# Kernel tuning notes

Hardware: AMD Instinct MI355X
Metric: run time of the kernel (lower is better)

## Reference

```python
import jax, jax.numpy as jnp
import numpy as np

B = 262144          # batch of sample points
L = 16              # hash levels
T = 1 << 19         # hash table size per level
F = 2               # features per level
BASE_RES = 16
FINEST_RES = 512
DH = 64             # density MLP hidden
DOUT = 16           # density MLP out (density_out dim)
CH = 64             # color MLP hidden
PRIMES = np.array([1, 2654435761, 805459861], dtype=np.uint32)
_b = np.exp((np.log(FINEST_RES) - np.log(BASE_RES)) / (L - 1))
RES = jnp.asarray(np.floor(BASE_RES * _b ** np.arange(L)).astype(np.float32))  # (L,)


def _linear_init(key, fan_in, fan_out):
    kw, kb = jax.random.split(key)
    bound = 1.0 / np.sqrt(fan_in)
    w = jax.random.uniform(kw, (fan_in, fan_out), minval=-bound, maxval=bound)
    b = jax.random.uniform(kb, (fan_out,), minval=-bound, maxval=bound)
    return w, b


def setup_inputs() -> dict:
    key = jax.random.key(0)
    ks = jax.random.split(key, 10)
    coords = jax.random.uniform(ks[0], (B, 3), dtype=jnp.float32)          # in [0,1]
    directions = jax.random.normal(ks[1], (B, 3), dtype=jnp.float32)
    embeddings = jax.random.uniform(ks[2], (L, T, F), minval=-1e-4, maxval=1e-4, dtype=jnp.float32)
    dw1, db1 = _linear_init(ks[3], L * F, DH)
    dw2, db2 = _linear_init(ks[4], DH, DOUT)
    cw1, cb1 = _linear_init(ks[5], 16 + DOUT, CH)
    cw2, cb2 = _linear_init(ks[6], CH, CH)
    cw3, cb3 = _linear_init(ks[7], CH, CH)
    cw4, cb4 = _linear_init(ks[8], CH, 3)
    return dict(coords=coords, directions=directions, embeddings=embeddings,
                dw1=dw1, db1=db1, dw2=dw2, db2=db2,
                cw1=cw1, cb1=cb1, cw2=cw2, cb2=cb2,
                cw3=cw3, cb3=cb3, cw4=cw4, cb4=cb4)


def hash_encode(coords, embeddings):
    # coords: (B,3) in [0,1]; embeddings: (L,T,F)
    pos = coords[:, None, :] * RES[None, :, None]            # (B,L,3)
    p0 = jnp.floor(pos)
    frac = pos - p0                                           # (B,L,3)
    p0 = p0.astype(jnp.uint32)
    corners = jnp.stack([p0, p0 + jnp.uint32(1)], axis=-1)    # (B,L,3,2)
    h_ax = corners * jnp.asarray(PRIMES)[None, None, :, None]  # uint32 wraparound
    hidx = (h_ax[:, :, 0, :, None, None]
            ^ h_ax[:, :, 1, None, :, None]
            ^ h_ax[:, :, 2, None, None, :])                   # (B,L,2,2,2)
    hidx = (hidx & jnp.uint32(T - 1)).reshape(coords.shape[0], L, 8).astype(jnp.int32)
    feats = embeddings[jnp.arange(L)[None, :, None], hidx]    # (B,L,8,F)
    wx = jnp.stack([1.0 - frac[..., 0], frac[..., 0]], -1)    # (B,L,2)
    wy = jnp.stack([1.0 - frac[..., 1], frac[..., 1]], -1)
    wz = jnp.stack([1.0 - frac[..., 2], frac[..., 2]], -1)
    w = (wx[:, :, :, None, None] * wy[:, :, None, :, None] * wz[:, :, None, None, :])
    w = w.reshape(coords.shape[0], L, 8)                      # (B,L,8)
    out = jnp.sum(feats * w[..., None], axis=2)               # (B,L,F)
    return out.reshape(coords.shape[0], L * F)


def sh_encode_deg4(d):
    # d: (B,3) unit directions in [-1,1]; degree-4 real SH basis (16 comps)
    x, y, z = d[:, 0], d[:, 1], d[:, 2]
    xx, yy, zz = x * x, y * y, z * z
    xy, yz, xz = x * y, y * z, x * z
    c = jnp.full_like(x, 0.28209479177387814)
    return jnp.stack([
        c,
        -0.48860251190291987 * y,
        0.48860251190291987 * z,
        -0.48860251190291987 * x,
        1.0925484305920792 * xy,
        -1.0925484305920792 * yz,
        0.94617469575755997 * zz - 0.31539156525251999,
        -1.0925484305920792 * xz,
        0.54627421529603959 * (xx - yy),
        0.59004358992664352 * y * (-3.0 * xx + yy),
        2.8906114426405538 * xy * z,
        0.45704579946446572 * y * (1.0 - 5.0 * zz),
        0.3731763325901154 * z * (5.0 * zz - 3.0),
        0.45704579946446572 * x * (1.0 - 5.0 * zz),
        1.4453057213202769 * z * (xx - yy),
        0.59004358992664352 * x * (xx - 3.0 * yy),
    ], axis=1)


def reference(coords, directions, embeddings, dw1, db1, dw2, db2,
              cw1, cb1, cw2, cb2, cw3, cb3, cw4, cb4):
    # density net: hash encode -> Linear+ReLU -> Linear
    feat = hash_encode(coords, embeddings)                    # (B, L*F)
    h = jax.nn.relu(feat @ dw1 + db1)
    density_out = h @ dw2 + db2                               # (B, DOUT)
    density = jnp.exp(density_out[:, 0])                      # TruncExp fwd = exp
    # color net
    d = directions / jnp.linalg.norm(directions, axis=1, keepdims=True)
    d01 = (d + 1.0) / 2.0                                     # remap as in module
    sh = sh_encode_deg4(d01 * 2.0 - 1.0)                      # encoder maps back to [-1,1]
    inp = jnp.concatenate([sh, density_out], axis=1)          # (B, 32)
    x = jax.nn.relu(inp @ cw1 + cb1)
    x = jax.nn.relu(x @ cw2 + cb2)
    x = jax.nn.relu(x @ cw3 + cb3)
    color = jax.nn.sigmoid(x @ cw4 + cb4)                     # (B, 3)
    return density, color
```

## Files before the change

### kernel.cpp

```cpp
#include <hip/hip_runtime.h>
#include <cmath>

#define NPTS 262144
#define NLVL 16
#define TBL  524288u
#define TMASK 524287u
#define TPB  256
#define NQ   7

typedef __attribute__((ext_vector_type(8))) short short8;
typedef __attribute__((ext_vector_type(4))) float f32x4;

struct ResArr { float r[NLVL]; };
struct QuadInfo { int off[NQ]; int dim[NQ]; };

__device__ __forceinline__ unsigned short f2bf(float f) {
    union { float f; unsigned u; } v; v.f = f;
    unsigned r = v.u + 0x7FFFu + ((v.u >> 16) & 1u);
    return (unsigned short)(r >> 16);
}
__device__ __forceinline__ float blo(unsigned u) {
    union { unsigned v; float f; } x; x.v = u << 16; return x.f;
}
__device__ __forceinline__ float bhi(unsigned u) {
    union { unsigned v; float f; } x; x.v = u & 0xffff0000u; return x.f;
}
__device__ __forceinline__ unsigned packbf(float a, float b) {
    return (unsigned)f2bf(a) | ((unsigned)f2bf(b) << 16);
}

#define MFMA(a,b,c) __builtin_amdgcn_mfma_f32_16x16x32_bf16((a),(b),(c),0,0,0)

__global__ __launch_bounds__(256) void prep_k(
    const float* __restrict__ emb,
    const float* __restrict__ coords,
    float4* __restrict__ c4,
    uint4* __restrict__ oct, QuadInfo qi,
    const float* __restrict__ dw1, const float* __restrict__ db1,
    const float* __restrict__ dw2, const float* __restrict__ db2,
    const float* __restrict__ cw1, const float* __restrict__ cb1,
    const float* __restrict__ cw2, const float* __restrict__ cb2,
    const float* __restrict__ cw3, const float* __restrict__ cb3,
    const float* __restrict__ cw4, const float* __restrict__ cb4,
    unsigned short* __restrict__ wpk, float* __restrict__ bpk)
{
    const int l = blockIdx.y;
    const int tid = threadIdx.x;

    if (l == 7) {
        if (blockIdx.x == 0) {
            const int wid  = tid >> 6;
            const int lane = tid & 63;
            const int m16  = lane & 15;
            const int q    = lane >> 4;
            const unsigned char MAT[28] = {0,0,0,0, 1,1, 2,2,2,2, 3,3,3,3,3,3,3,3, 4,4,4,4,4,4,4,4, 5,5};
            const unsigned char K0 [28] = {0,0,0,0, 0,32, 0,0,0,0, 0,0,0,0,32,32,32,32, 0,0,0,0,32,32,32,32, 0,32};
            const unsigned char N0 [28] = {0,16,32,48, 0,0, 0,16,32,48, 0,16,32,48,0,16,32,48, 0,16,32,48,0,16,32,48, 0,0};
            #pragma unroll
            for (int s = 0; s < 28; ++s) {
                if ((s & 3) == wid) {
                    const int mat = MAT[s];
                    const float* src = mat==0?dw1 : mat==1?dw2 : mat==2?cw1 : mat==3?cw2 : mat==4?cw3 : cw4;
                    const int fan = (mat==1) ? 16 : (mat==5) ? 3 : 64;
                    const int k = (int)K0[s] + q*8;
                    const int n = (int)N0[s] + m16;
                    unsigned short u[8];
                    #pragma unroll
                    for (int j = 0; j < 8; ++j) {
                        float v = 0.f;
                        if (mat != 5 || n < 3) v = src[(k+j)*fan + n];
                        u[j] = f2bf(v);
                    }
                    unsigned* w32 = (unsigned*)(wpk + s*512 + lane*8);
                    w32[0] = (unsigned)u[0] | ((unsigned)u[1] << 16);
                    w32[1] = (unsigned)u[2] | ((unsigned)u[3] << 16);
                    w32[2] = (unsigned)u[4] | ((unsigned)u[5] << 16);
                    w32[3] = (unsigned)u[6] | ((unsigned)u[7] << 16);
                }
            }
            {
                int t = tid;
                if      (t <  64) bpk[t] = db1[t];
                else if (t <  80) bpk[t] = db2[t-64];
                else if (t < 144) bpk[t] = cb1[t-80];
                else if (t < 208) bpk[t] = cb2[t-144];
            }
            if (tid < 80) {
                int t = tid + 208;
                if (t < 272) bpk[t] = cb3[t-208];
                else         bpk[t] = (t-272 < 3) ? cb4[t-272] : 0.f;
            }
        } else if (blockIdx.x <= 1024) {
            const int p = (blockIdx.x - 1) * 256 + tid;
            float4 c;
            c.x = coords[3*p]; c.y = coords[3*p+1]; c.z = coords[3*p+2]; c.w = 0.f;
            c4[p] = c;
        }
        return;
    }

    const int t = blockIdx.x * 256 + tid;
    const int D = qi.dim[l];
    if (t >= D*D*D) return;
    const int DD = D*D;
    const unsigned z = (unsigned)t % (unsigned)D;
    const unsigned rem = (unsigned)t / (unsigned)D;
    const unsigned y = rem % (unsigned)D;

    const float2* __restrict__ emb2 = (const float2*)emb;
    const unsigned base = (unsigned)l * TBL;
    const unsigned x = rem / (unsigned)D;
    const unsigned hy0 = y*2654435761u, hy1 = (y+1u)*2654435761u;
    const unsigned hz0 = z*805459861u,  hz1 = (z+1u)*805459861u;

    const float2 a = emb2[base + ((x^hy0^hz0)&TMASK)];
    const float2 b = emb2[base + ((x^hy0^hz1)&TMASK)];
    const float2 c = emb2[base + ((x^hy1^hz0)&TMASK)];
    const float2 d = emb2[base + ((x^hy1^hz1)&TMASK)];

    uint4 q;
    q.x = packbf(a.x, a.y);
    q.y = packbf(b.x, b.y);
    q.z = packbf(c.x, c.y);
    q.w = packbf(d.x, d.y);

    const int e = qi.off[l] + t;
    oct[2*e] = q;
    if (t >= DD)
        oct[2*(e - DD) + 1] = q;
}

__global__ __launch_bounds__(256) void hash_encode_k(
    const float4* __restrict__ c4,
    const float* __restrict__ emb,
    const uint4* __restrict__ oct,
    unsigned* __restrict__ featws,
    ResArr res, QuadInfo qi)
{
    const int tid = threadIdx.x;
    const int b   = blockIdx.x;
    const int xcd = b & 7;
    const int s   = b >> 3;

    if (s < 1152) {
        int l, p;
        if (s < 1024) {
            l = 7 + xcd;
            p = s * 256 + tid;
        } else {
            l = 15;
            p = xcd * 32768 + (s - 1024) * 256 + tid;
        }

        const float4 cc = c4[p];
        const float r = res.r[l];
        const float px = cc.x*r, py = cc.y*r, pz = cc.z*r;
        const float fpx = floorf(px), fpy = floorf(py), fpz = floorf(pz);
        const float fx = px-fpx, fy = py-fpy, fz = pz-fpz;
        const unsigned ix=(unsigned)fpx, iy=(unsigned)fpy, iz=(unsigned)fpz;
        const unsigned hy0=iy*2654435761u, hy1=(iy+1u)*2654435761u;
        const unsigned hz0=iz*805459861u,  hz1=(iz+1u)*805459861u;
        const unsigned base  = (unsigned)l * TBL;
        const unsigned base4 = (unsigned)l * (TBL >> 1);
        const float2* __restrict__ emb2 = (const float2*)emb;
        const float4* __restrict__ emb4 = (const float4*)emb;

        const unsigned m = ix ^ (ix + 1u);
        const unsigned h00 = (ix^hy0^hz0) & TMASK;
        const unsigned h01 = (ix^hy0^hz1) & TMASK;
        const unsigned h10 = (ix^hy1^hz0) & TMASK;
        const unsigned h11 = (ix^hy1^hz1) & TMASK;

        const float4 p00 = emb4[base4 + (h00 >> 1)];
        const float4 p01 = emb4[base4 + (h01 >> 1)];
        const float4 p10 = emb4[base4 + (h10 >> 1)];
        const float4 p11 = emb4[base4 + (h11 >> 1)];

        float2 f000, f001, f010, f011, f100, f101, f110, f111;
        f000.x = (h00&1) ? p00.z : p00.x;  f000.y = (h00&1) ? p00.w : p00.y;
        f001.x = (h01&1) ? p01.z : p01.x;  f001.y = (h01&1) ? p01.w : p01.y;
        f010.x = (h10&1) ? p10.z : p10.x;  f010.y = (h10&1) ? p10.w : p10.y;
        f011.x = (h11&1) ? p11.z : p11.x;  f011.y = (h11&1) ? p11.w : p11.y;
        f100.x = (h00&1) ? p00.x : p00.z;  f100.y = (h00&1) ? p00.y : p00.w;
        f101.x = (h01&1) ? p01.x : p01.z;  f101.y = (h01&1) ? p01.y : p01.w;
        f110.x = (h10&1) ? p10.x : p10.z;  f110.y = (h10&1) ? p10.y : p10.w;
        f111.x = (h11&1) ? p11.x : p11.z;  f111.y = (h11&1) ? p11.y : p11.w;

        if (m != 1u) {
            f100 = emb2[base + ((h00 ^ m) & TMASK)];
            f101 = emb2[base + ((h01 ^ m) & TMASK)];
            f110 = emb2[base + ((h10 ^ m) & TMASK)];
            f111 = emb2[base + ((h11 ^ m) & TMASK)];
        }

        const float wx0=1.f-fx, wy0=1.f-fy, wz0=1.f-fz;
        float o0, o1;
        o0 = wx0*wy0*wz0*f000.x;                 o1 = wx0*wy0*wz0*f000.y;
        o0 = fmaf(wx0*wy0*fz,  f001.x, o0);      o1 = fmaf(wx0*wy0*fz,  f001.y, o1);
        o0 = fmaf(wx0*fy*wz0,  f010.x, o0);      o1 = fmaf(wx0*fy*wz0,  f010.y, o1);
        o0 = fmaf(wx0*fy*fz,   f011.x, o0);      o1 = fmaf(wx0*fy*fz,   f011.y, o1);
        o0 = fmaf(fx*wy0*wz0,  f100.x, o0);      o1 = fmaf(fx*wy0*wz0,  f100.y, o1);
        o0 = fmaf(fx*wy0*fz,   f101.x, o0);      o1 = fmaf(fx*wy0*fz,   f101.y, o1);
        o0 = fmaf(fx*fy*wz0,   f110.x, o0);      o1 = fmaf(fx*fy*wz0,   f110.y, o1);
        o0 = fmaf(fx*fy*fz,    f111.x, o0);      o1 = fmaf(fx*fy*fz,    f111.y, o1);

        featws[(size_t)l * NPTS + p] = packbf(o0, o1);
    } else {
        const int g  = xcd * 224 + (s - 1152);
        const int l  = g >> 8;
        const int c  = g & 255;
        const int D  = qi.dim[l];
        const int off = qi.off[l];
        const float r = res.r[l];

        int   pidx[4];
        uint4 qA[4], qB[4];
        float fxa[4], fya[4], fza[4];
        #pragma unroll
        for (int k = 0; k < 4; ++k) {
            const int p = c*1024 + k*256 + tid;
            pidx[k] = p;
            const float4 cc = c4[p];
            const float px = cc.x*r, py = cc.y*r, pz = cc.z*r;
            const float fpx = floorf(px), fpy = floorf(py), fpz = floorf(pz);
            fxa[k] = px-fpx; fya[k] = py-fpy; fza[k] = pz-fpz;
            const int ix=(int)fpx, iy=(int)fpy, iz=(int)fpz;
            const int v0 = off + (ix*D + iy)*D + iz;
            qA[k] = oct[2*v0];
            qB[k] = oct[2*v0 + 1];
        }
        #pragma unroll
        for (int k = 0; k < 4; ++k) {
            const float fx = fxa[k], fy = fya[k], fz = fza[k];
            const float wx0=1.f-fx, wy0=1.f-fy, wz0=1.f-fz;
            const float w000=wx0*wy0*wz0, w001=wx0*wy0*fz;
            const float w010=wx0*fy*wz0,  w011=wx0*fy*fz;
            const float w100=fx*wy0*wz0,  w101=fx*wy0*fz;
            const float w110=fx*fy*wz0,   w111=fx*fy*fz;
            float o0, o1;
            o0 = w000*blo(qA[k].x);              o1 = w000*bhi(qA[k].x);
            o0 = fmaf(w001, blo(qA[k].y), o0);   o1 = fmaf(w001, bhi(qA[k].y), o1);
            o0 = fmaf(w010, blo(qA[k].z), o0);   o1 = fmaf(w010, bhi(qA[k].z), o1);
            o0 = fmaf(w011, blo(qA[k].w), o0);   o1 = fmaf(w011, bhi(qA[k].w), o1);
            o0 = fmaf(w100, blo(qB[k].x), o0);   o1 = fmaf(w100, bhi(qB[k].x), o1);
            o0 = fmaf(w101, blo(qB[k].y), o0);   o1 = fmaf(w101, bhi(qB[k].y), o1);
            o0 = fmaf(w110, blo(qB[k].z), o0);   o1 = fmaf(w110, bhi(qB[k].z), o1);
            o0 = fmaf(w111, blo(qB[k].w), o0);   o1 = fmaf(w111, bhi(qB[k].w), o1);
            featws[(size_t)l * NPTS + pidx[k]] = packbf(o0, o1);
        }
    }
}

__global__ __launch_bounds__(256, 4) void mlp_mfma_k(
    const unsigned* __restrict__ featws,
    const unsigned short* __restrict__ wpk,
    const float* __restrict__ bpk,
    const float* __restrict__ dirs,
    float* __restrict__ out)
{
    const int tid  = threadIdx.x;
    const int wid  = tid >> 6;
    const int lane = tid & 63;
    const int m16  = lane & 15;
    const int q    = lane >> 4;

    __shared__ __align__(16) unsigned short wlds[28 * 512];
    __shared__ float blds[288];
    __shared__ __align__(16) unsigned short actL[4 * 16 * 72];

    {
        uint4* dst = (uint4*)wlds;
        const uint4* srcv = (const uint4*)wpk;
        #pragma unroll
        for (int j = 0; j < 7; ++j) dst[j*256 + tid] = srcv[j*256 + tid];
        if (tid < 256) blds[tid] = bpk[tid];
        if (tid < 32)  blds[256 + tid] = bpk[256 + tid];
    }
    __syncthreads();

    const int pbase = blockIdx.x * TPB;

    unsigned short* aw = actL + wid*1152;
    const short8* wfr = (const short8*)wlds;

    #pragma unroll 1
    for (int iter = 0; iter < 4; ++iter) {
        const int tile = wid + 4*iter;
        const int loc0 = tile*16;
        const int p0g  = pbase + loc0;

        union { unsigned u[4]; short8 s; } af;
        #pragma unroll
        for (int j = 0; j < 4; ++j)
            af.u[j] = featws[(size_t)(q*4 + j) * NPTS + p0g + m16];
        const short8 a0 = af.s;

        f32x4 acc[4];
        #pragma unroll
        for (int nc = 0; nc < 4; ++nc) {
            const float b = blds[nc*16 + m16];
            acc[nc] = (f32x4){b,b,b,b};
            acc[nc] = MFMA(a0, wfr[nc*64 + lane], acc[nc]);
        }
        #pragma unroll
        for (int nc = 0; nc < 4; ++nc)
            #pragma unroll
            for (int r = 0; r < 4; ++r)
                aw[(q*4+r)*72 + nc*16 + m16] = f2bf(fmaxf(acc[nc][r], 0.f));

        short8 ad0 = *(const short8*)(aw + m16*72 + q*8);
        short8 ad1 = *(const short8*)(aw + m16*72 + 32 + q*8);
        f32x4 dob;
        { const float b = blds[64 + m16]; dob = (f32x4){b,b,b,b}; }
        dob = MFMA(ad0, wfr[4*64 + lane], dob);
        dob = MFMA(ad1, wfr[5*64 + lane], dob);

        if (m16 == 0) {
            #pragma unroll
            for (int r = 0; r < 4; ++r) out[p0g + q*4 + r] = expf(dob[r]);
        }

        #pragma unroll
        for (int r = 0; r < 4; ++r)
            aw[(q*4+r)*72 + 16 + m16] = f2bf(dob[r]);
        {
            const int pg = p0g + m16;
            const float dx0 = dirs[3*pg], dy0 = dirs[3*pg+1], dz0 = dirs[3*pg+2];
            const float inv = 1.f / sqrtf(dx0*dx0 + dy0*dy0 + dz0*dz0);
            float x = dx0*inv, y = dy0*inv, z = dz0*inv;
            x = ((x+1.f)*0.5f)*2.f - 1.f;
            y = ((y+1.f)*0.5f)*2.f - 1.f;
            z = ((z+1.f)*0.5f)*2.f - 1.f;
            float s0, s1, s2, s3;
            switch (q) {
            case 0: s0 = 0.28209479177387814f;
                    s1 = -0.48860251190291987f*y;
                    s2 =  0.48860251190291987f*z;
                    s3 = -0.48860251190291987f*x; break;
            case 1: s0 =  1.0925484305920792f*x*y;
                    s1 = -1.0925484305920792f*y*z;
                    s2 =  0.94617469575756f*z*z - 0.31539156525252f;
                    s3 = -1.0925484305920792f*x*z; break;
            case 2: s0 =  0.5462742152960396f*(x*x - y*y);
                    s1 =  0.5900435899266435f*y*(-3.f*x*x + y*y);
                    s2 =  2.890611442640554f*x*y*z;
                    s3 =  0.4570457994644657f*y*(1.f - 5.f*z*z); break;
            default:s0 =  0.3731763325901154f*z*(5.f*z*z - 3.f);
                    s1 =  0.4570457994644657f*x*(1.f - 5.f*z*z);
                    s2 =  1.445305721320277f*z*(x*x - y*y);
                    s3 =  0.5900435899266435f*x*(x*x - 3.f*y*y); break;
            }
            unsigned* ip = (unsigned*)(aw + m16*72 + q*4);
            ip[0] = packbf(s0, s1);
            ip[1] = packbf(s2, s3);
        }

        short8 ac0 = *(const short8*)(aw + m16*72 + q*8);
        #pragma unroll
        for (int nc = 0; nc < 4; ++nc) {
            const float b = blds[80 + nc*16 + m16];
            acc[nc] = (f32x4){b,b,b,b};
            acc[nc] = MFMA(ac0, wfr[(6+nc)*64 + lane], acc[nc]);
        }
        #pragma unroll
        for (int nc = 0; nc < 4; ++nc)
            #pragma unroll
            for (int r = 0; r < 4; ++r)
                aw[(q*4+r)*72 + nc*16 + m16] = f2bf(fmaxf(acc[nc][r], 0.f));

        short8 a20 = *(const short8*)(aw + m16*72 + q*8);
        short8 a21 = *(const short8*)(aw + m16*72 + 32 + q*8);
        #pragma unroll
        for (int nc = 0; nc < 4; ++nc) {
            const float b = blds[144 + nc*16 + m16];
            acc[nc] = (f32x4){b,b,b,b};
            acc[nc] = MFMA(a20, wfr[(10+nc)*64 + lane], acc[nc]);
            acc[nc] = MFMA(a21, wfr[(14+nc)*64 + lane], acc[nc]);
        }
        #pragma unroll
        for (int nc = 0; nc < 4; ++nc)
            #pragma unroll
            for (int r = 0; r < 4; ++r)
                aw[(q*4+r)*72 + nc*16 + m16] = f2bf(fmaxf(acc[nc][r], 0.f));

        short8 a30 = *(const short8*)(aw + m16*72 + q*8);
        short8 a31 = *(const short8*)(aw + m16*72 + 32 + q*8);
        #pragma unroll
        for (int nc = 0; nc < 4; ++nc) {
            const float b = blds[208 + nc*16 + m16];
            acc[nc] = (f32x4){b,b,b,b};
            acc[nc] = MFMA(a30, wfr[(18+nc)*64 + lane], acc[nc]);
            acc[nc] = MFMA(a31, wfr[(22+nc)*64 + lane], acc[nc]);
        }
        #pragma unroll
        for (int nc = 0; nc < 4; ++nc)
            #pragma unroll
            for (int r = 0; r < 4; ++r)
                aw[(q*4+r)*72 + nc*16 + m16] = f2bf(fmaxf(acc[nc][r], 0.f));

        short8 a40 = *(const short8*)(aw + m16*72 + q*8);
        short8 a41 = *(const short8*)(aw + m16*72 + 32 + q*8);
        f32x4 c4v;
        { const float b = blds[272 + m16]; c4v = (f32x4){b,b,b,b}; }
        c4v = MFMA(a40, wfr[26*64 + lane], c4v);
        c4v = MFMA(a41, wfr[27*64 + lane], c4v);
        if (m16 < 3) {
            #pragma unroll
            for (int r = 0; r < 4; ++r)
                out[NPTS + 3*(p0g + q*4 + r) + m16] = 1.f / (1.f + expf(-c4v[r]));
        }
    }
}

extern "C" void kernel_launch(void* const* d_in, const int* in_sizes, int n_in,
                              void* d_out, int out_size, void* d_ws, size_t ws_size,
                              hipStream_t stream)
{
    ResArr res;
    const double b = exp((log(512.0) - log(16.0)) / 15.0);
    for (int l = 0; l < NLVL; ++l)
        res.r[l] = (float)floor(16.0 * pow(b, (double)l));

    QuadInfo qi;
    int off = 0, maxn = 0;
    for (int l = 0; l < NQ; ++l) {
        const int D = (int)res.r[l] + 1;
        qi.dim[l] = D;
        qi.off[l] = off;
        off += D*D*D;
        if (D*D*D > maxn) maxn = D*D*D;
    }

    unsigned*       featws = (unsigned*)d_ws;
    uint4*          oct    = (uint4*)((char*)d_ws + (size_t)NLVL * NPTS * 4);
    float4*         c4     = (float4*)((char*)oct + (size_t)off * 32);
    unsigned short* wpk    = (unsigned short*)((char*)c4 + (size_t)NPTS * 16);
    float*          bpk    = (float*)((char*)wpk + 28 * 512 * 2);

    prep_k<<<dim3((maxn + 255)/256, 8), 256, 0, stream>>>(
        (const float*)d_in[2],
        (const float*)d_in[0],
        c4, oct, qi,
        (const float*)d_in[3],  (const float*)d_in[4],
        (const float*)d_in[5],  (const float*)d_in[6],
        (const float*)d_in[7],  (const float*)d_in[8],
        (const float*)d_in[9],  (const float*)d_in[10],
        (const float*)d_in[11], (const float*)d_in[12],
        (const float*)d_in[13], (const float*)d_in[14],
        wpk, bpk);

    hash_encode_k<<<11008, 256, 0, stream>>>(
        c4,
        (const float*)d_in[2],
        oct, featws, res, qi);

    mlp_mfma_k<<<NPTS/TPB, 256, 0, stream>>>(
        featws, wpk, bpk,
        (const float*)d_in[1],
        (float*)d_out);
}
```

Baseline: 239.5 us.

## Fuse coarse-level octant interpolation into MLP kernel and merge prep with hash encode

The separate prep and hash-encode kernels are merged into one launch. The fine-level hash lookups and the dense coarse-level octant table build now run as different block ranges of that single grid. The coarse levels 0-6 are no longer interpolated in a separate pass that writes features to global memory. Instead the MLP kernel reads the bf16 octant table directly and interpolates into shared memory, and the float4 coords repack buffer is dropped. This removes a launch and a global round trip for seven feature levels. In exchange the MLP kernel uses more shared memory and registers, with launch bounds lowered from 4 to 3, and the fine-level blocks now do strided coordinate loads.

```diff
diff --git a/kernel.cpp b/kernel.cpp
--- a/kernel.cpp
+++ b/kernel.cpp
@@ -31,24 +31,128 @@
 
 #define MFMA(a,b,c) __builtin_amdgcn_mfma_f32_16x16x32_bf16((a),(b),(c),0,0,0)
 
-__global__ __launch_bounds__(256) void prep_k(
+__global__ __launch_bounds__(256) void fused_encode_k(
+    const float* __restrict__ coords,
     const float* __restrict__ emb,
-    const float* __restrict__ coords,
-    float4* __restrict__ c4,
-    uint4* __restrict__ oct, QuadInfo qi,
+    uint4* __restrict__ oct,
+    unsigned* __restrict__ featws,
     const float* __restrict__ dw1, const float* __restrict__ db1,
     const float* __restrict__ dw2, const float* __restrict__ db2,
     const float* __restrict__ cw1, const float* __restrict__ cb1,
     const float* __restrict__ cw2, const float* __restrict__ cb2,
     const float* __restrict__ cw3, const float* __restrict__ cb3,
     const float* __restrict__ cw4, const float* __restrict__ cb4,
-    unsigned short* __restrict__ wpk, float* __restrict__ bpk)
+    unsigned short* __restrict__ wpk, float* __restrict__ bpk,
+    ResArr res, QuadInfo qi, int ncell, int ncb, int tailn)
 {
-    const int l = blockIdx.y;
     const int tid = threadIdx.x;
-
-    if (l == 7) {
-        if (blockIdx.x == 0) {
+    const int b   = blockIdx.x;
+    const int xcd = b & 7;
+    const int s   = b >> 3;
+
+    if (s < 1152) {
+        int l, p;
+        if (s < 1024) {
+            l = 7 + xcd;
+            p = s * 256 + tid;
+        } else {
+            l = 15;
+            p = xcd * 32768 + (s - 1024) * 256 + tid;
+        }
+
+        const float cx = coords[3*p], cy = coords[3*p+1], cz = coords[3*p+2];
+        const float r = res.r[l];
+        const float px = cx*r, py = cy*r, pz = cz*r;
+        const float fpx = floorf(px), fpy = floorf(py), fpz = floorf(pz);
+        const float fx = px-fpx, fy = py-fpy, fz = pz-fpz;
+        const unsigned ix=(unsigned)fpx, iy=(unsigned)fpy, iz=(unsigned)fpz;
+        const unsigned hy0=iy*2654435761u, hy1=(iy+1u)*2654435761u;
+        const unsigned hz0=iz*805459861u,  hz1=(iz+1u)*805459861u;
+        const unsigned base  = (unsigned)l * TBL;
+        const unsigned base4 = (unsigned)l * (TBL >> 1);
+        const float2* __restrict__ emb2 = (const float2*)emb;
+        const float4* __restrict__ emb4 = (const float4*)emb;
+
+        const unsigned m = ix ^ (ix + 1u);
+        const unsigned h00 = (ix^hy0^hz0) & TMASK;
+        const unsigned h01 = (ix^hy0^hz1) & TMASK;
+        const unsigned h10 = (ix^hy1^hz0) & TMASK;
+        const unsigned h11 = (ix^hy1^hz1) & TMASK;
+
+        const float4 p00 = emb4[base4 + (h00 >> 1)];
+        const float4 p01 = emb4[base4 + (h01 >> 1)];
+        const float4 p10 = emb4[base4 + (h10 >> 1)];
+        const float4 p11 = emb4[base4 + (h11 >> 1)];
+
+        float2 f000, f001, f010, f011, f100, f101, f110, f111;
+        f000.x = (h00&1) ? p00.z : p00.x;  f000.y = (h00&1) ? p00.w : p00.y;
+        f001.x = (h01&1) ? p01.z : p01.x;  f001.y = (h01&1) ? p01.w : p01.y;
+        f010.x = (h10&1) ? p10.z : p10.x;  f010.y = (h10&1) ? p10.w : p10.y;
+        f011.x = (h11&1) ? p11.z : p11.x;  f011.y = (h11&1) ? p11.w : p11.y;
+        f100.x = (h00&1) ? p00.x : p00.z;  f100.y = (h00&1) ? p00.y : p00.w;
+        f101.x = (h01&1) ? p01.x : p01.z;  f101.y = (h01&1) ? p01.y : p01.w;
+        f110.x = (h10&1) ? p10.x : p10.z;  f110.y = (h10&1) ? p10.y : p10.w;
+        f111.x = (h11&1) ? p11.x : p11.z;  f111.y = (h11&1) ? p11.y : p11.w;
+
+        if (m != 1u) {
+            f100 = emb2[base + ((h00 ^ m) & TMASK)];
+            f101 = emb2[base + ((h01 ^ m) & TMASK)];
+            f110 = emb2[base + ((h10 ^ m) & TMASK)];
+            f111 = emb2[base + ((h11 ^ m) & TMASK)];
+        }
+
+        const float wx0=1.f-fx, wy0=1.f-fy, wz0=1.f-fz;
+        float o0, o1;
+        o0 = wx0*wy0*wz0*f000.x;                 o1 = wx0*wy0*wz0*f000.y;
+        o0 = fmaf(wx0*wy0*fz,  f001.x, o0);      o1 = fmaf(wx0*wy0*fz,  f001.y, o1);
+        o0 = fmaf(wx0*fy*wz0,  f010.x, o0);      o1 = fmaf(wx0*fy*wz0,  f010.y, o1);
+        o0 = fmaf(wx0*fy*fz,   f011.x, o0);      o1 = fmaf(wx0*fy*fz,   f011.y, o1);
+        o0 = fmaf(fx*wy0*wz0,  f100.x, o0);      o1 = fmaf(fx*wy0*wz0,  f100.y, o1);
+        o0 = fmaf(fx*wy0*fz,   f101.x, o0);      o1 = fmaf(fx*wy0*fz,   f101.y, o1);
+        o0 = fmaf(fx*fy*wz0,   f110.x, o0);      o1 = fmaf(fx*fy*wz0,   f110.y, o1);
+        o0 = fmaf(fx*fy*fz,    f111.x, o0);      o1 = fmaf(fx*fy*fz,    f111.y, o1);
+
+        featws[(size_t)l * NPTS + p] = packbf(o0, o1);
+    } else {
+        const int rank = xcd * tailn + (s - 1152);
+        if (rank < ncb) {
+            const int gcell = rank * 256 + tid;
+            if (gcell >= ncell) return;
+
+            int l = 0;
+            #pragma unroll
+            for (int j = 1; j < NQ; ++j) if (gcell >= qi.off[j]) l = j;
+            const int off = qi.off[l];
+            const int D   = qi.dim[l];
+            const int t   = gcell - off;
+            const int DD  = D*D;
+
+            const unsigned z = (unsigned)t % (unsigned)D;
+            const unsigned rem = (unsigned)t / (unsigned)D;
+            const unsigned y = rem % (unsigned)D;
+            const unsigned x = rem / (unsigned)D;
+
+            const float2* __restrict__ emb2 = (const float2*)emb;
+            const unsigned base = (unsigned)l * TBL;
+            const unsigned hy0 = y*2654435761u, hy1 = (y+1u)*2654435761u;
+            const unsigned hz0 = z*805459861u,  hz1 = (z+1u)*805459861u;
+
+            const float2 a = emb2[base + ((x^hy0^hz0)&TMASK)];
+            const float2 bb= emb2[base + ((x^hy0^hz1)&TMASK)];
+            const float2 c = emb2[base + ((x^hy1^hz0)&TMASK)];
+            const float2 d = emb2[base + ((x^hy1^hz1)&TMASK)];
+
+            uint4 q;
+            q.x = packbf(a.x, a.y);
+            q.y = packbf(bb.x, bb.y);
+            q.z = packbf(c.x, c.y);
+            q.w = packbf(d.x, d.y);
+
+            const int e = off + t;
+            oct[2*e] = q;
+            if (t >= DD)
+                oct[2*(e - DD) + 1] = q;
+        } else if (rank == ncb) {
             const int wid  = tid >> 6;
             const int lane = tid & 63;
             const int m16  = lane & 15;
@@ -57,13 +161,13 @@
             const unsigned char K0 [28] = {0,0,0,0, 0,32, 0,0,0,0, 0,0,0,0,32,32,32,32, 0,0,0,0,32,32,32,32, 0,32};
             const unsigned char N0 [28] = {0,16,32,48, 0,0, 0,16,32,48, 0,16,32,48,0,16,32,48, 0,16,32,48,0,16,32,48, 0,0};
             #pragma unroll
-            for (int s = 0; s < 28; ++s) {
-                if ((s & 3) == wid) {
-                    const int mat = MAT[s];
+            for (int s2 = 0; s2 < 28; ++s2) {
+                if ((s2 & 3) == wid) {
+                    const int mat = MAT[s2];
                     const float* src = mat==0?dw1 : mat==1?dw2 : mat==2?cw1 : mat==3?cw2 : mat==4?cw3 : cw4;
                     const int fan = (mat==1) ? 16 : (mat==5) ? 3 : 64;
-                    const int k = (int)K0[s] + q*8;
-                    const int n = (int)N0[s] + m16;
+                    const int k = (int)K0[s2] + q*8;
+                    const int n = (int)N0[s2] + m16;
                     unsigned short u[8];
                     #pragma unroll
                     for (int j = 0; j < 8; ++j) {
@@ -71,7 +175,7 @@
                         if (mat != 5 || n < 3) v = src[(k+j)*fan + n];
                         u[j] = f2bf(v);
                     }
-                    unsigned* w32 = (unsigned*)(wpk + s*512 + lane*8);
+                    unsigned* w32 = (unsigned*)(wpk + s2*512 + lane*8);
                     w32[0] = (unsigned)u[0] | ((unsigned)u[1] << 16);
                     w32[1] = (unsigned)u[2] | ((unsigned)u[3] << 16);
                     w32[2] = (unsigned)u[4] | ((unsigned)u[5] << 16);
@@ -90,195 +194,74 @@
                 if (t < 272) bpk[t] = cb3[t-208];
                 else         bpk[t] = (t-272 < 3) ? cb4[t-272] : 0.f;
             }
-        } else if (blockIdx.x <= 1024) {
-            const int p = (blockIdx.x - 1) * 256 + tid;
-            float4 c;
-            c.x = coords[3*p]; c.y = coords[3*p+1]; c.z = coords[3*p+2]; c.w = 0.f;
-            c4[p] = c;
-        }
-        return;
+        }
     }
-
-    const int t = blockIdx.x * 256 + tid;
-    const int D = qi.dim[l];
-    if (t >= D*D*D) return;
-    const int DD = D*D;
-    const unsigned z = (unsigned)t % (unsigned)D;
-    const unsigned rem = (unsigned)t / (unsigned)D;
-    const unsigned y = rem % (unsigned)D;
-
-    const float2* __restrict__ emb2 = (const float2*)emb;
-    const unsigned base = (unsigned)l * TBL;
-    const unsigned x = rem / (unsigned)D;
-    const unsigned hy0 = y*2654435761u, hy1 = (y+1u)*2654435761u;
-    const unsigned hz0 = z*805459861u,  hz1 = (z+1u)*805459861u;
-
-    const float2 a = emb2[base + ((x^hy0^hz0)&TMASK)];
-    const float2 b = emb2[base + ((x^hy0^hz1)&TMASK)];
-    const float2 c = emb2[base + ((x^hy1^hz0)&TMASK)];
-    const float2 d = emb2[base + ((x^hy1^hz1)&TMASK)];
-
-    uint4 q;
-    q.x = packbf(a.x, a.y);
-    q.y = packbf(b.x, b.y);
-    q.z = packbf(c.x, c.y);
-    q.w = packbf(d.x, d.y);
-
-    const int e = qi.off[l] + t;
-    oct[2*e] = q;
-    if (t >= DD)
-        oct[2*(e - DD) + 1] = q;
-}
-
-__global__ __launch_bounds__(256) void hash_encode_k(
-    const float4* __restrict__ c4,
-    const float* __restrict__ emb,
+}
+
+__global__ __launch_bounds__(256, 3) void mlp_mfma_k(
+    const unsigned* __restrict__ featws,
     const uint4* __restrict__ oct,
-    unsigned* __restrict__ featws,
+    const float* __restrict__ coords,
+    const unsigned short* __restrict__ wpk,
+    const float* __restrict__ bpk,
+    const float* __restrict__ dirs,
+    float* __restrict__ out,
     ResArr res, QuadInfo qi)
 {
-    const int tid = threadIdx.x;
-    const int b   = blockIdx.x;
-    const int xcd = b & 7;
-    const int s   = b >> 3;
-
-    if (s < 1152) {
-        int l, p;
-        if (s < 1024) {
-            l = 7 + xcd;
-            p = s * 256 + tid;
-        } else {
-            l = 15;
-            p = xcd * 32768 + (s - 1024) * 256 + tid;
-        }
-
-        const float4 cc = c4[p];
-        const float r = res.r[l];
-        const float px = cc.x*r, py = cc.y*r, pz = cc.z*r;
-        const float fpx = floorf(px), fpy = floorf(py), fpz = floorf(pz);
-        const float fx = px-fpx, fy = py-fpy, fz = pz-fpz;
-        const unsigned ix=(unsigned)fpx, iy=(unsigned)fpy, iz=(unsigned)fpz;
-        const unsigned hy0=iy*2654435761u, hy1=(iy+1u)*2654435761u;
-        const unsigned hz0=iz*805459861u,  hz1=(iz+1u)*805459861u;
-        const unsigned base  = (unsigned)l * TBL;
-        const unsigned base4 = (unsigned)l * (TBL >> 1);
-        const float2* __restrict__ emb2 = (const float2*)emb;
-        const float4* __restrict__ emb4 = (const float4*)emb;
-
-        const unsigned m = ix ^ (ix + 1u);
-        const unsigned h00 = (ix^hy0^hz0) & TMASK;
-        const unsigned h01 = (ix^hy0^hz1) & TMASK;
-        const unsigned h10 = (ix^hy1^hz0) & TMASK;
-        const unsigned h11 = (ix^hy1^hz1) & TMASK;
-
-        const float4 p00 = emb4[base4 + (h00 >> 1)];
-        const float4 p01 = emb4[base4 + (h01 >> 1)];
-        const float4 p10 = emb4[base4 + (h10 >> 1)];
-        const float4 p11 = emb4[base4 + (h11 >> 1)];
-
-        float2 f000, f001, f010, f011, f100, f101, f110, f111;
-        f000.x = (h00&1) ? p00.z : p00.x;  f000.y = (h00&1) ? p00.w : p00.y;
-        f001.x = (h01&1) ? p01.z : p01.x;  f001.y = (h01&1) ? p01.w : p01.y;
-        f010.x = (h10&1) ? p10.z : p10.x;  f010.y = (h10&1) ? p10.w : p10.y;
-        f011.x = (h11&1) ? p11.z : p11.x;  f011.y = (h11&1) ? p11.w : p11.y;
-        f100.x = (h00&1) ? p00.x : p00.z;  f100.y = (h00&1) ? p00.y : p00.w;
-        f101.x = (h01&1) ? p01.x : p01.z;  f101.y = (h01&1) ? p01.y : p01.w;
-        f110.x = (h10&1) ? p10.x : p10.z;  f110.y = (h10&1) ? p10.y : p10.w;
-        f111.x = (h11&1) ? p11.x : p11.z;  f111.y = (h11&1) ? p11.y : p11.w;
-
-        if (m != 1u) {
-            f100 = emb2[base + ((h00 ^ m) & TMASK)];
-            f101 = emb2[base + ((h01 ^ m) & TMASK)];
-            f110 = emb2[base + ((h10 ^ m) & TMASK)];
-            f111 = emb2[base + ((h11 ^ m) & TMASK)];
-        }
-
-        const float wx0=1.f-fx, wy0=1.f-fy, wz0=1.f-fz;
-        float o0, o1;
-        o0 = wx0*wy0*wz0*f000.x;                 o1 = wx0*wy0*wz0*f000.y;
-        o0 = fmaf(wx0*wy0*fz,  f001.x, o0);      o1 = fmaf(wx0*wy0*fz,  f001.y, o1);
-        o0 = fmaf(wx0*fy*wz0,  f010.x, o0);      o1 = fmaf(wx0*fy*wz0,  f010.y, o1);
-        o0 = fmaf(wx0*fy*fz,   f011.x, o0);      o1 = fmaf(wx0*fy*fz,   f011.y, o1);
-        o0 = fmaf(fx*wy0*wz0,  f100.x, o0);      o1 = fmaf(fx*wy0*wz0,  f100.y, o1);
-        o0 = fmaf(fx*wy0*fz,   f101.x, o0);      o1 = fmaf(fx*wy0*fz,   f101.y, o1);
-        o0 = fmaf(fx*fy*wz0,   f110.x, o0);      o1 = fmaf(fx*fy*wz0,   f110.y, o1);
-        o0 = fmaf(fx*fy*fz,    f111.x, o0);      o1 = fmaf(fx*fy*fz,    f111.y, o1);
-
-        featws[(size_t)l * NPTS + p] = packbf(o0, o1);
-    } else {
-        const int g  = xcd * 224 + (s - 1152);
-        const int l  = g >> 8;
-        const int c  = g & 255;
-        const int D  = qi.dim[l];
-        const int off = qi.off[l];
-        const float r = res.r[l];
-
-        int   pidx[4];
-        uint4 qA[4], qB[4];
-        float fxa[4], fya[4], fza[4];
-        #pragma unroll
-        for (int k = 0; k < 4; ++k) {
-            const int p = c*1024 + k*256 + tid;
-            pidx[k] = p;
-            const float4 cc = c4[p];
-            const float px = cc.x*r, py = cc.y*r, pz = cc.z*r;
+    const int tid  = threadIdx.x;
+    const int wid  = tid >> 6;
+    const int lane = tid & 63;
+    const int m16  = lane & 15;
+    const int q    = lane >> 4;
+
+    __shared__ __align__(16) unsigned short wlds[28 * 512];
+    __shared__ float blds[288];
+    __shared__ __align__(16) unsigned short actL[4 * 16 * 72];
+    __shared__ unsigned featO[256 * 8];
+
+    {
+        uint4* dst = (uint4*)wlds;
+        const uint4* srcv = (const uint4*)wpk;
+        #pragma unroll
+        for (int j = 0; j < 7; ++j) dst[j*256 + tid] = srcv[j*256 + tid];
+        if (tid < 256) blds[tid] = bpk[tid];
+        if (tid < 32)  blds[256 + tid] = bpk[256 + tid];
+    }
+
+    const int pbase = blockIdx.x * TPB;
+
+    {
+        const int p = pbase + tid;
+        const float cx = coords[3*p], cy = coords[3*p+1], cz = coords[3*p+2];
+        #pragma unroll
+        for (int l = 0; l < NQ; ++l) {
+            const float r = res.r[l];
+            const float px = cx*r, py = cy*r, pz = cz*r;
             const float fpx = floorf(px), fpy = floorf(py), fpz = floorf(pz);
-            fxa[k] = px-fpx; fya[k] = py-fpy; fza[k] = pz-fpz;
+            const float fx = px-fpx, fy = py-fpy, fz = pz-fpz;
             const int ix=(int)fpx, iy=(int)fpy, iz=(int)fpz;
-            const int v0 = off + (ix*D + iy)*D + iz;
-            qA[k] = oct[2*v0];
-            qB[k] = oct[2*v0 + 1];
-        }
-        #pragma unroll
-        for (int k = 0; k < 4; ++k) {
-            const float fx = fxa[k], fy = fya[k], fz = fza[k];
+            const int D = qi.dim[l];
+            const int v0 = qi.off[l] + (ix*D + iy)*D + iz;
+            const uint4 qA = oct[2*v0];
+            const uint4 qB = oct[2*v0 + 1];
             const float wx0=1.f-fx, wy0=1.f-fy, wz0=1.f-fz;
             const float w000=wx0*wy0*wz0, w001=wx0*wy0*fz;
             const float w010=wx0*fy*wz0,  w011=wx0*fy*fz;
             const float w100=fx*wy0*wz0,  w101=fx*wy0*fz;
             const float w110=fx*fy*wz0,   w111=fx*fy*fz;
             float o0, o1;
-            o0 = w000*blo(qA[k].x);              o1 = w000*bhi(qA[k].x);
-            o0 = fmaf(w001, blo(qA[k].y), o0);   o1 = fmaf(w001, bhi(qA[k].y), o1);
-            o0 = fmaf(w010, blo(qA[k].z), o0);   o1 = fmaf(w010, bhi(qA[k].z), o1);
-            o0 = fmaf(w011, blo(qA[k].w), o0);   o1 = fmaf(w011, bhi(qA[k].w), o1);
-            o0 = fmaf(w100, blo(qB[k].x), o0);   o1 = fmaf(w100, bhi(qB[k].x), o1);
-            o0 = fmaf(w101, blo(qB[k].y), o0);   o1 = fmaf(w101, bhi(qB[k].y), o1);
-            o0 = fmaf(w110, blo(qB[k].z), o0);   o1 = fmaf(w110, bhi(qB[k].z), o1);
-            o0 = fmaf(w111, blo(qB[k].w), o0);   o1 = fmaf(w111, bhi(qB[k].w), o1);
-            featws[(size_t)l * NPTS + pidx[k]] = packbf(o0, o1);
-        }
-    }
-}
-
-__global__ __launch_bounds__(256, 4) void mlp_mfma_k(
-    const unsigned* __restrict__ featws,
-    const unsigned short* __restrict__ wpk,
-    const float* __restrict__ bpk,
-    const float* __restrict__ dirs,
-    float* __restrict__ out)
-{
-    const int tid  = threadIdx.x;
-    const int wid  = tid >> 6;
-    const int lane = tid & 63;
-    const int m16  = lane & 15;
-    const int q    = lane >> 4;
-
-    __shared__ __align__(16) unsigned short wlds[28 * 512];
-    __shared__ float blds[288];
-    __shared__ __align__(16) unsigned short actL[4 * 16 * 72];
-
-    {
-        uint4* dst = (uint4*)wlds;
-        const uint4* srcv = (const uint4*)wpk;
-        #pragma unroll
-        for (int j = 0; j < 7; ++j) dst[j*256 + tid] = srcv[j*256 + tid];
-        if (tid < 256) blds[tid] = bpk[tid];
-        if (tid < 32)  blds[256 + tid] = bpk[256 + tid];
+            o0 = w000*blo(qA.x);              o1 = w000*bhi(qA.x);
+            o0 = fmaf(w001, blo(qA.y), o0);   o1 = fmaf(w001, bhi(qA.y), o1);
+            o0 = fmaf(w010, blo(qA.z), o0);   o1 = fmaf(w010, bhi(qA.z), o1);
+            o0 = fmaf(w011, blo(qA.w), o0);   o1 = fmaf(w011, bhi(qA.w), o1);
+            o0 = fmaf(w100, blo(qB.x), o0);   o1 = fmaf(w100, bhi(qB.x), o1);
+            o0 = fmaf(w101, blo(qB.y), o0);   o1 = fmaf(w101, bhi(qB.y), o1);
+            o0 = fmaf(w110, blo(qB.z), o0);   o1 = fmaf(w110, bhi(qB.z), o1);
+            o0 = fmaf(w111, blo(qB.w), o0);   o1 = fmaf(w111, bhi(qB.w), o1);
+            featO[tid*8 + l] = packbf(o0, o1);
+        }
     }
     __syncthreads();
-
-    const int pbase = blockIdx.x * TPB;
 
     unsigned short* aw = actL + wid*1152;
     const short8* wfr = (const short8*)wlds;
@@ -291,8 +274,11 @@
 
         union { unsigned u[4]; short8 s; } af;
         #pragma unroll
-        for (int j = 0; j < 4; ++j)
-            af.u[j] = featws[(size_t)(q*4 + j) * NPTS + p0g + m16];
+        for (int j = 0; j < 4; ++j) {
+            const int lvl = q*4 + j;
+            af.u[j] = (lvl < NQ) ? featO[(loc0+m16)*8 + lvl]
+                                 : featws[(size_t)lvl * NPTS + p0g + m16];
+        }
         const short8 a0 = af.s;
 
         f32x4 acc[4];
@@ -422,40 +408,40 @@
         res.r[l] = (float)floor(16.0 * pow(b, (double)l));
 
     QuadInfo qi;
-    int off = 0, maxn = 0;
+    int ncell = 0;
     for (int l = 0; l < NQ; ++l) {
         const int D = (int)res.r[l] + 1;
         qi.dim[l] = D;
-        qi.off[l] = off;
-        off += D*D*D;
-        if (D*D*D > maxn) maxn = D*D*D;
+        qi.off[l] = ncell;
+        ncell += D*D*D;
     }
+    const int ncb   = (ncell + 255) / 256;
+    const int tailn = (ncb + 1 + 7) / 8;
+    const int smax  = 1152 + tailn;
+    const int grid  = smax * 8;
 
     unsigned*       featws = (unsigned*)d_ws;
     uint4*          oct    = (uint4*)((char*)d_ws + (size_t)NLVL * NPTS * 4);
-    float4*         c4     = (float4*)((char*)oct + (size_t)off * 32);
-    unsigned short* wpk    = (unsigned short*)((char*)c4 + (size_t)NPTS * 16);
+    unsigned short* wpk    = (unsigned short*)((char*)oct + (size_t)ncell * 32);
     float*          bpk    = (float*)((char*)wpk + 28 * 512 * 2);
 
-    prep_k<<<dim3((maxn + 255)/256, 8), 256, 0, stream>>>(
+    fused_encode_k<<<grid, 256, 0, stream>>>(
+        (const float*)d_in[0],
         (const float*)d_in[2],
-        (const float*)d_in[0],
-        c4, oct, qi,
+        oct, featws,
         (const float*)d_in[3],  (const float*)d_in[4],
         (const float*)d_in[5],  (const float*)d_in[6],
         (const float*)d_in[7],  (const float*)d_in[8],
         (const float*)d_in[9],  (const float*)d_in[10],
         (const float*)d_in[11], (const float*)d_in[12],
         (const float*)d_in[13], (const float*)d_in[14],
-        wpk, bpk);
-
-    hash_encode_k<<<11008, 256, 0, stream>>>(
-        c4,
-        (const float*)d_in[2],
-        oct, featws, res, qi);
+        wpk, bpk, res, qi, ncell, ncb, tailn);
 
     mlp_mfma_k<<<NPTS/TPB, 256, 0, stream>>>(
-        featws, wpk, bpk,
+        featws, oct,
+        (const float*)d_in[0],
+        wpk, bpk,
         (const float*)d_in[1],
-        (float*)d_out);
-}
+        (float*)d_out,
+        res, qi);
+}
```

Measured after the change: 229.6 us. -4.2%, faster.
